# Optimization experiments

Hardware: AMD Instinct MI355X
Metric: run time of the kernel (lower is better)

## Reference

```python
import jax, jax.numpy as jnp
import numpy as np

C_ATOM = 128
N_HEADS = 4
HEAD_DIM = C_ATOM // N_HEADS


def setup_inputs() -> dict:
    key = jax.random.key(0)
    ks = jax.random.split(key, 11)
    B, L, A = 16, 4096, 4
    x = jax.random.normal(ks[0], (B, L, A, C_ATOM), dtype=jnp.float32)
    mask = jax.random.randint(ks[1], (B, L, A), 0, 2) > 0
    mask = mask.at[..., 0].set(True)  # ensure >=1 valid atom per residue (avoids all--inf softmax)
    s = 1.0 / np.sqrt(C_ATOM)
    def lin(k):
        kw, kb = jax.random.split(k)
        W = jax.random.uniform(kw, (C_ATOM, C_ATOM), jnp.float32, -s, s)
        b = jax.random.uniform(kb, (C_ATOM,), jnp.float32, -s, s)
        return W, b
    Wq, bq = lin(ks[2])
    Wk, bk = lin(ks[3])
    Wv, bv = lin(ks[4])
    Wo, bo = lin(ks[5])
    return {"x": x, "mask": mask, "Wq": Wq, "bq": bq, "Wk": Wk, "bk": bk,
            "Wv": Wv, "bv": bv, "Wo": Wo, "bo": bo}


def reference(x, mask, Wq, bq, Wk, bk, Wv, bv, Wo, bo):
    B, L, A, C = x.shape
    H, D = N_HEADS, HEAD_DIM
    # q/k/v projections (torch Linear: x @ W.T + b)
    q = (x @ Wq.T + bq).reshape(B, L, A, H, D)
    k = (x @ Wk.T + bk).reshape(B, L, A, H, D)
    v = (x @ Wv.T + bv).reshape(B, L, A, H, D)
    scale = 1.0 / jnp.sqrt(jnp.asarray(D, x.dtype))
    # per-residue 4x4 attention scores: [B, L, H, q_atom, k_atom]
    scores = jnp.einsum("blqhd,blkhd->blhqk", q, k) * scale
    # key-side mask bias (broadcast over heads and query atoms)
    bias = jnp.where(mask[:, :, None, None, :], 0.0, -jnp.inf).astype(x.dtype)
    attn = jax.nn.softmax(scores + bias, axis=-1)
    out = jnp.einsum("blhqk,blkhd->blqhd", attn, v).reshape(B, L, A, C)
    out = out @ Wo.T + bo
    residue_mask = jnp.any(mask, axis=-1)[..., None, None].astype(out.dtype)  # [B,L,1,1]
    return out * residue_mask
```

## Files before the change

kernel.cpp:

```cpp
#include <hip/hip_runtime.h>
#include <stdint.h>


typedef __bf16 bf16x8 __attribute__((ext_vector_type(8)));
typedef float  f32x4  __attribute__((ext_vector_type(4)));

#define N_RES 65536
#define RPB   16
#define MROWS 64
#define CDIM  128

__device__ __forceinline__ uint32_t pk2(float a, float b) {
    uint32_t ua = __builtin_bit_cast(uint32_t, a) + 0x8000u;
    uint32_t ub = __builtin_bit_cast(uint32_t, b) + 0x8000u;
    return (ua >> 16) | (ub & 0xffff0000u);
}
__device__ __forceinline__ uint16_t f2bf(float a) {
    uint32_t u = __builtin_bit_cast(uint32_t, a);
    return (uint16_t)((u + 0x7fffu + ((u >> 16) & 1u)) >> 16);
}
__device__ __forceinline__ bf16x8 pack8(float4 f0, float4 f1) {
    uint4 uu = make_uint4(pk2(f0.x, f0.y), pk2(f0.z, f0.w),
                          pk2(f1.x, f1.y), pk2(f1.z, f1.w));
    return __builtin_bit_cast(bf16x8, uu);
}
__device__ __forceinline__ void bf8_unpack(uint4 u, float* f) {
    f[0] = __builtin_bit_cast(float, u.x << 16);
    f[1] = __builtin_bit_cast(float, u.x & 0xffff0000u);
    f[2] = __builtin_bit_cast(float, u.y << 16);
    f[3] = __builtin_bit_cast(float, u.y & 0xffff0000u);
    f[4] = __builtin_bit_cast(float, u.z << 16);
    f[5] = __builtin_bit_cast(float, u.z & 0xffff0000u);
    f[6] = __builtin_bit_cast(float, u.w << 16);
    f[7] = __builtin_bit_cast(float, u.w & 0xffff0000u);
}

__global__ void wconv_kernel(const float* __restrict__ wq, const float* __restrict__ wk,
                             const float* __restrict__ wv, const float* __restrict__ wo,
                             uint16_t* __restrict__ dst) {
    int i = blockIdx.x * 256 + threadIdx.x;
    const float* s = (i < 16384) ? wq : (i < 32768) ? wk : (i < 49152) ? wv : wo;
    dst[i] = f2bf(s[i & 16383]);
}

template <bool USEWS>
__global__ __launch_bounds__(256, 2)
void laa_main(const float* __restrict__ x, const int* __restrict__ mask,
              const float* __restrict__ Wq, const float* __restrict__ bq,
              const float* __restrict__ Wk, const float* __restrict__ bk,
              const float* __restrict__ Wv, const float* __restrict__ bv,
              const float* __restrict__ Wo, const float* __restrict__ bo,
              const uint16_t* __restrict__ wbf,
              float* __restrict__ out) {
    __shared__ uint16_t sQ[MROWS * CDIM];
    __shared__ uint16_t sK[MROWS * CDIM];
    __shared__ uint16_t sV[MROWS * CDIM];
    __shared__ uint16_t sO[MROWS * CDIM];

    const int tid  = threadIdx.x;
    const int wave = tid >> 6;
    const int lane = tid & 63;
    const int lrow = lane & 15;
    const int quad = lane >> 4;
    const long m0  = (long)blockIdx.x * MROWS;

    const f32x4 vzero = {0.f, 0.f, 0.f, 0.f};

    bf16x8 af[4][4];
    {
        const float* xb = x + m0 * CDIM;
        #pragma unroll
        for (int m = 0; m < 4; ++m) {
            const float* rowp = xb + (m * 16 + lrow) * CDIM;
            #pragma unroll
            for (int ks = 0; ks < 4; ++ks) {
                const float4* p = (const float4*)(rowp + ks * 32 + quad * 8);
                af[m][ks] = pack8(p[0], p[1]);
            }
        }
    }

    f32x4 acc[3][4][2];
    #pragma unroll
    for (int g = 0; g < 3; ++g)
        #pragma unroll
        for (int m = 0; m < 4; ++m)
            #pragma unroll
            for (int nt = 0; nt < 2; ++nt) acc[g][m][nt] = vzero;

    const float* wsrc32[3] = {Wq, Wk, Wv};
    #pragma unroll
    for (int ks = 0; ks < 4; ++ks) {
        bf16x8 bfr[3][2];
        #pragma unroll
        for (int g = 0; g < 3; ++g) {
            #pragma unroll
            for (int nt = 0; nt < 2; ++nt) {
                int wrow = wave * 32 + nt * 16 + lrow;
                if constexpr (USEWS) {
                    bfr[g][nt] = *(const bf16x8*)(wbf + g * 16384 + wrow * CDIM + ks * 32 + quad * 8);
                } else {
                    const float* wp = wsrc32[g] + wrow * CDIM + ks * 32 + quad * 8;
                    bfr[g][nt] = pack8(((const float4*)wp)[0], ((const float4*)wp)[1]);
                }
            }
        }
        #pragma unroll
        for (int g = 0; g < 3; ++g)
            #pragma unroll
            for (int m = 0; m < 4; ++m)
                #pragma unroll
                for (int nt = 0; nt < 2; ++nt)
                    acc[g][m][nt] = __builtin_amdgcn_mfma_f32_16x16x32_bf16(
                        af[m][ks], bfr[g][nt], acc[g][m][nt], 0, 0, 0);
    }

    {
        uint16_t* sdst[3] = {sQ, sK, sV};
        const float* bias[3] = {bq, bk, bv};
        #pragma unroll
        for (int g = 0; g < 3; ++g) {
            #pragma unroll
            for (int nt = 0; nt < 2; ++nt) {
                int col = wave * 32 + nt * 16 + lrow;
                float bb = bias[g][col];
                #pragma unroll
                for (int m = 0; m < 4; ++m) {
                    #pragma unroll
                    for (int r = 0; r < 4; ++r) {
                        int row = m * 16 + quad * 4 + r;
                        sdst[g][row * CDIM + col] = f2bf(acc[g][m][nt][r] + bb);
                    }
                }
            }
        }
    }
    __syncthreads();

    {
        const int rl = tid >> 4;
        const int h  = (tid >> 2) & 3;
        const int qa = tid & 3;
        const int rowq = rl * 4 + qa;
        const int cb = h * 32;

        const int4 mk = *(const int4*)(mask + ((long)blockIdx.x * RPB + rl) * 4);
        const int mka[4] = {mk.x, mk.y, mk.z, mk.w};

        float qv[32];
        {
            const uint4* qp = (const uint4*)(sQ + rowq * CDIM + cb);
            #pragma unroll
            for (int c = 0; c < 4; ++c) bf8_unpack(qp[c], qv + c * 8);
        }
        float sc[4];
        #pragma unroll
        for (int ka = 0; ka < 4; ++ka) {
            const uint4* kp = (const uint4*)(sK + (rl * 4 + ka) * CDIM + cb);
            float d = 0.f;
            #pragma unroll
            for (int c = 0; c < 4; ++c) {
                float kv[8]; bf8_unpack(kp[c], kv);
                #pragma unroll
                for (int j = 0; j < 8; ++j) d += qv[c * 8 + j] * kv[j];
            }
            sc[ka] = d * 0.17677669529663689f;
        }
        float mx = -3e38f;
        #pragma unroll
        for (int ka = 0; ka < 4; ++ka) if (mka[ka]) mx = fmaxf(mx, sc[ka]);
        float e[4], ssum = 0.f;
        #pragma unroll
        for (int ka = 0; ka < 4; ++ka) {
            e[ka] = mka[ka] ? __expf(sc[ka] - mx) : 0.f;
            ssum += e[ka];
        }
        const float inv = ssum > 0.f ? 1.f / ssum : 0.f;

        float o[32];
        #pragma unroll
        for (int j = 0; j < 32; ++j) o[j] = 0.f;
        #pragma unroll
        for (int ka = 0; ka < 4; ++ka) {
            float wgt = e[ka] * inv;
            const uint4* vp = (const uint4*)(sV + (rl * 4 + ka) * CDIM + cb);
            #pragma unroll
            for (int c = 0; c < 4; ++c) {
                float vv[8]; bf8_unpack(vp[c], vv);
                #pragma unroll
                for (int j = 0; j < 8; ++j) o[c * 8 + j] += wgt * vv[j];
            }
        }
        uint32_t* op = (uint32_t*)(sO + rowq * CDIM + cb);
        #pragma unroll
        for (int c2 = 0; c2 < 16; ++c2) op[c2] = pk2(o[2 * c2], o[2 * c2 + 1]);
    }
    __syncthreads();

    f32x4 acc2[4][2];
    #pragma unroll
    for (int m = 0; m < 4; ++m)
        #pragma unroll
        for (int nt = 0; nt < 2; ++nt) acc2[m][nt] = vzero;

    #pragma unroll
    for (int ks = 0; ks < 4; ++ks) {
        bf16x8 a2[4];
        #pragma unroll
        for (int m = 0; m < 4; ++m)
            a2[m] = *(const bf16x8*)(sO + (m * 16 + lrow) * CDIM + ks * 32 + quad * 8);
        bf16x8 b2[2];
        #pragma unroll
        for (int nt = 0; nt < 2; ++nt) {
            int wrow = wave * 32 + nt * 16 + lrow;
            if constexpr (USEWS) {
                b2[nt] = *(const bf16x8*)(wbf + 3 * 16384 + wrow * CDIM + ks * 32 + quad * 8);
            } else {
                const float* wp = Wo + wrow * CDIM + ks * 32 + quad * 8;
                b2[nt] = pack8(((const float4*)wp)[0], ((const float4*)wp)[1]);
            }
        }
        #pragma unroll
        for (int m = 0; m < 4; ++m)
            #pragma unroll
            for (int nt = 0; nt < 2; ++nt)
                acc2[m][nt] = __builtin_amdgcn_mfma_f32_16x16x32_bf16(
                    a2[m], b2[nt], acc2[m][nt], 0, 0, 0);
    }
    {
        #pragma unroll
        for (int m = 0; m < 4; ++m) {
            const int4 mk2 = *(const int4*)(mask + ((long)blockIdx.x * RPB + m * 4 + quad) * 4);
            const float rm = (mk2.x | mk2.y | mk2.z | mk2.w) ? 1.f : 0.f;
            #pragma unroll
            for (int nt = 0; nt < 2; ++nt) {
                int col = wave * 32 + nt * 16 + lrow;
                float bb = bo[col];
                #pragma unroll
                for (int r = 0; r < 4; ++r) {
                    long row = m0 + m * 16 + quad * 4 + r;
                    out[row * CDIM + col] = (acc2[m][nt][r] + bb) * rm;
                }
            }
        }
    }
}

extern "C" void kernel_launch(void* const* d_in, const int* in_sizes, int n_in,
                              void* d_out, int out_size, void* d_ws, size_t ws_size,
                              hipStream_t stream) {
    const float* x    = (const float*)d_in[0];
    const int*   mask = (const int*)d_in[1];
    const float* Wq   = (const float*)d_in[2];
    const float* bq   = (const float*)d_in[3];
    const float* Wk   = (const float*)d_in[4];
    const float* bk   = (const float*)d_in[5];
    const float* Wv   = (const float*)d_in[6];
    const float* bv   = (const float*)d_in[7];
    const float* Wo   = (const float*)d_in[8];
    const float* bo   = (const float*)d_in[9];
    float* out = (float*)d_out;

    const int nblocks = N_RES / RPB;
    const bool usews = ws_size >= (size_t)(4 * 16384 * sizeof(uint16_t));
    if (usews) {
        uint16_t* wbf = (uint16_t*)d_ws;
        wconv_kernel<<<256, 256, 0, stream>>>(Wq, Wk, Wv, Wo, wbf);
        laa_main<true><<<nblocks, 256, 0, stream>>>(x, mask, Wq, bq, Wk, bk, Wv, bv,
                                                    Wo, bo, wbf, out);
    } else {
        laa_main<false><<<nblocks, 256, 0, stream>>>(x, mask, Wq, bq, Wk, bk, Wv, bv,
                                                     Wo, bo, nullptr, out);
    }
}
```

Baseline: 329.1 us.

## Keep per-head attention in registers via MFMA, switch to fp16, drop Q/K/V LDS

Each wave now owns one head's 32 columns and computes Q^T, K^T and V tiles directly in MFMA accumulator layout. Scores come from an MFMA on the transposed Q/K tiles, and the value mix is a block-diagonal 16x16x16 MFMA. This removes the sQ/sK/sV shared buffers, one barrier and the scalar dot-product attention phase. Precision changes from bf16 to fp16 with round-toward-zero packing, LDS use drops to one padded buffer, and launch bounds rise to 3 blocks per SM, at some risk of fp16 range and precision issues.

```diff
diff --git a/kernel.cpp b/kernel.cpp
--- a/kernel.cpp
+++ b/kernel.cpp
@@ -2,37 +2,21 @@
 #include <stdint.h>
 
 
-typedef __bf16 bf16x8 __attribute__((ext_vector_type(8)));
-typedef float  f32x4  __attribute__((ext_vector_type(4)));
+typedef __fp16 f16;
+typedef f16   f16x2 __attribute__((ext_vector_type(2)));
+typedef f16   f16x4 __attribute__((ext_vector_type(4)));
+typedef f16   f16x8 __attribute__((ext_vector_type(8)));
+typedef float f32x4 __attribute__((ext_vector_type(4)));
 
 #define N_RES 65536
 #define RPB   16
 #define MROWS 64
 #define CDIM  128
-
-__device__ __forceinline__ uint32_t pk2(float a, float b) {
-    uint32_t ua = __builtin_bit_cast(uint32_t, a) + 0x8000u;
-    uint32_t ub = __builtin_bit_cast(uint32_t, b) + 0x8000u;
-    return (ua >> 16) | (ub & 0xffff0000u);
-}
-__device__ __forceinline__ uint16_t f2bf(float a) {
-    uint32_t u = __builtin_bit_cast(uint32_t, a);
-    return (uint16_t)((u + 0x7fffu + ((u >> 16) & 1u)) >> 16);
-}
-__device__ __forceinline__ bf16x8 pack8(float4 f0, float4 f1) {
-    uint4 uu = make_uint4(pk2(f0.x, f0.y), pk2(f0.z, f0.w),
-                          pk2(f1.x, f1.y), pk2(f1.z, f1.w));
-    return __builtin_bit_cast(bf16x8, uu);
-}
-__device__ __forceinline__ void bf8_unpack(uint4 u, float* f) {
-    f[0] = __builtin_bit_cast(float, u.x << 16);
-    f[1] = __builtin_bit_cast(float, u.x & 0xffff0000u);
-    f[2] = __builtin_bit_cast(float, u.y << 16);
-    f[3] = __builtin_bit_cast(float, u.y & 0xffff0000u);
-    f[4] = __builtin_bit_cast(float, u.z << 16);
-    f[5] = __builtin_bit_cast(float, u.z & 0xffff0000u);
-    f[6] = __builtin_bit_cast(float, u.w << 16);
-    f[7] = __builtin_bit_cast(float, u.w & 0xffff0000u);
+#define SOP   136
+
+__device__ __forceinline__ uint32_t pkh(float a, float b) {
+    f16x2 h = __builtin_amdgcn_cvt_pkrtz(a, b);
+    return __builtin_bit_cast(uint32_t, h);
 }
 
 __global__ void wconv_kernel(const float* __restrict__ wq, const float* __restrict__ wk,
@@ -40,11 +24,26 @@
                              uint16_t* __restrict__ dst) {
     int i = blockIdx.x * 256 + threadIdx.x;
     const float* s = (i < 16384) ? wq : (i < 32768) ? wk : (i < 49152) ? wv : wo;
-    dst[i] = f2bf(s[i & 16383]);
+    f16 h = (f16)s[i & 16383];
+    dst[i] = __builtin_bit_cast(uint16_t, h);
 }
 
 template <bool USEWS>
-__global__ __launch_bounds__(256, 2)
+__device__ __forceinline__ f16x8 ldw16(const uint16_t* __restrict__ wbf,
+                                       const float* __restrict__ w32,
+                                       int goff, int row, int col) {
+    if constexpr (USEWS) {
+        return *(const f16x8*)(wbf + goff + row * CDIM + col);
+    } else {
+        const float4* p = (const float4*)(w32 + row * CDIM + col);
+        float4 a = p[0], b = p[1];
+        uint4 u = make_uint4(pkh(a.x, a.y), pkh(a.z, a.w), pkh(b.x, b.y), pkh(b.z, b.w));
+        return __builtin_bit_cast(f16x8, u);
+    }
+}
+
+template <bool USEWS>
+__global__ __launch_bounds__(256, 3)
 void laa_main(const float* __restrict__ x, const int* __restrict__ mask,
               const float* __restrict__ Wq, const float* __restrict__ bq,
               const float* __restrict__ Wk, const float* __restrict__ bk,
@@ -52,151 +51,112 @@
               const float* __restrict__ Wo, const float* __restrict__ bo,
               const uint16_t* __restrict__ wbf,
               float* __restrict__ out) {
-    __shared__ uint16_t sQ[MROWS * CDIM];
-    __shared__ uint16_t sK[MROWS * CDIM];
-    __shared__ uint16_t sV[MROWS * CDIM];
-    __shared__ uint16_t sO[MROWS * CDIM];
+    __shared__ uint16_t sO[MROWS * SOP];
 
     const int tid  = threadIdx.x;
     const int wave = tid >> 6;
     const int lane = tid & 63;
-    const int lrow = lane & 15;
+    const int l15  = lane & 15;
     const int quad = lane >> 4;
+    const int hb   = wave * 32;
     const long m0  = (long)blockIdx.x * MROWS;
 
     const f32x4 vzero = {0.f, 0.f, 0.f, 0.f};
 
-    bf16x8 af[4][4];
-    {
-        const float* xb = x + m0 * CDIM;
+    f32x4 qt[4][2], kt[4][2], vv[4][2];
+    #pragma unroll
+    for (int m = 0; m < 4; ++m)
+        #pragma unroll
+        for (int n = 0; n < 2; ++n) { qt[m][n] = vzero; kt[m][n] = vzero; vv[m][n] = vzero; }
+
+    #pragma unroll
+    for (int ks = 0; ks < 4; ++ks) {
+        f16x8 xf[4];
         #pragma unroll
         for (int m = 0; m < 4; ++m) {
-            const float* rowp = xb + (m * 16 + lrow) * CDIM;
-            #pragma unroll
-            for (int ks = 0; ks < 4; ++ks) {
-                const float4* p = (const float4*)(rowp + ks * 32 + quad * 8);
-                af[m][ks] = pack8(p[0], p[1]);
-            }
-        }
-    }
-
-    f32x4 acc[3][4][2];
-    #pragma unroll
-    for (int g = 0; g < 3; ++g)
-        #pragma unroll
-        for (int m = 0; m < 4; ++m)
-            #pragma unroll
-            for (int nt = 0; nt < 2; ++nt) acc[g][m][nt] = vzero;
-
-    const float* wsrc32[3] = {Wq, Wk, Wv};
-    #pragma unroll
-    for (int ks = 0; ks < 4; ++ks) {
-        bf16x8 bfr[3][2];
-        #pragma unroll
-        for (int g = 0; g < 3; ++g) {
+            const float4* p = (const float4*)(x + (m0 + m * 16 + l15) * CDIM + ks * 32 + quad * 8);
+            float4 a = p[0], b = p[1];
+            uint4 u = make_uint4(pkh(a.x, a.y), pkh(a.z, a.w), pkh(b.x, b.y), pkh(b.z, b.w));
+            xf[m] = __builtin_bit_cast(f16x8, u);
+        }
+        f16x8 wqf[2], wkf[2], wvf[2];
+        #pragma unroll
+        for (int nt = 0; nt < 2; ++nt) {
+            int row = hb + nt * 16 + l15, col = ks * 32 + quad * 8;
+            wqf[nt] = ldw16<USEWS>(wbf, Wq, 0,     row, col);
+            wkf[nt] = ldw16<USEWS>(wbf, Wk, 16384, row, col);
+            wvf[nt] = ldw16<USEWS>(wbf, Wv, 32768, row, col);
+        }
+        #pragma unroll
+        for (int m = 0; m < 4; ++m) {
             #pragma unroll
             for (int nt = 0; nt < 2; ++nt) {
-                int wrow = wave * 32 + nt * 16 + lrow;
-                if constexpr (USEWS) {
-                    bfr[g][nt] = *(const bf16x8*)(wbf + g * 16384 + wrow * CDIM + ks * 32 + quad * 8);
-                } else {
-                    const float* wp = wsrc32[g] + wrow * CDIM + ks * 32 + quad * 8;
-                    bfr[g][nt] = pack8(((const float4*)wp)[0], ((const float4*)wp)[1]);
-                }
+                qt[m][nt] = __builtin_amdgcn_mfma_f32_16x16x32_f16(wqf[nt], xf[m], qt[m][nt], 0, 0, 0);
+                kt[m][nt] = __builtin_amdgcn_mfma_f32_16x16x32_f16(wkf[nt], xf[m], kt[m][nt], 0, 0, 0);
+                vv[m][nt] = __builtin_amdgcn_mfma_f32_16x16x32_f16(xf[m], wvf[nt], vv[m][nt], 0, 0, 0);
             }
         }
-        #pragma unroll
-        for (int g = 0; g < 3; ++g)
-            #pragma unroll
-            for (int m = 0; m < 4; ++m)
-                #pragma unroll
-                for (int nt = 0; nt < 2; ++nt)
-                    acc[g][m][nt] = __builtin_amdgcn_mfma_f32_16x16x32_bf16(
-                        af[m][ks], bfr[g][nt], acc[g][m][nt], 0, 0, 0);
-    }
-
-    {
-        uint16_t* sdst[3] = {sQ, sK, sV};
-        const float* bias[3] = {bq, bk, bv};
-        #pragma unroll
-        for (int g = 0; g < 3; ++g) {
-            #pragma unroll
-            for (int nt = 0; nt < 2; ++nt) {
-                int col = wave * 32 + nt * 16 + lrow;
-                float bb = bias[g][col];
-                #pragma unroll
-                for (int m = 0; m < 4; ++m) {
-                    #pragma unroll
-                    for (int r = 0; r < 4; ++r) {
-                        int row = m * 16 + quad * 4 + r;
-                        sdst[g][row * CDIM + col] = f2bf(acc[g][m][nt][r] + bb);
-                    }
-                }
-            }
+    }
+
+    const float s = 0.17677669529663689f;
+    float bqs[8], bks[8];
+    #pragma unroll
+    for (int nd = 0; nd < 2; ++nd) {
+        float4 q4 = *(const float4*)(bq + hb + nd * 16 + quad * 4);
+        float4 k4 = *(const float4*)(bk + hb + nd * 16 + quad * 4);
+        bqs[nd * 4 + 0] = q4.x * s; bqs[nd * 4 + 1] = q4.y * s;
+        bqs[nd * 4 + 2] = q4.z * s; bqs[nd * 4 + 3] = q4.w * s;
+        bks[nd * 4 + 0] = k4.x;     bks[nd * 4 + 1] = k4.y;
+        bks[nd * 4 + 2] = k4.z;     bks[nd * 4 + 3] = k4.w;
+    }
+    const float bvv0 = bv[hb + l15], bvv1 = bv[hb + 16 + l15];
+
+    float rm[4];
+    const bool diag = (quad == (l15 >> 2));
+    #pragma unroll
+    for (int m = 0; m < 4; ++m) {
+        uint4 uq, uk;
+        uq.x = pkh(qt[m][0][0] * s + bqs[0], qt[m][0][1] * s + bqs[1]);
+        uq.y = pkh(qt[m][0][2] * s + bqs[2], qt[m][0][3] * s + bqs[3]);
+        uq.z = pkh(qt[m][1][0] * s + bqs[4], qt[m][1][1] * s + bqs[5]);
+        uq.w = pkh(qt[m][1][2] * s + bqs[6], qt[m][1][3] * s + bqs[7]);
+        uk.x = pkh(kt[m][0][0] + bks[0], kt[m][0][1] + bks[1]);
+        uk.y = pkh(kt[m][0][2] + bks[2], kt[m][0][3] + bks[3]);
+        uk.z = pkh(kt[m][1][0] + bks[4], kt[m][1][1] + bks[5]);
+        uk.w = pkh(kt[m][1][2] + bks[6], kt[m][1][3] + bks[7]);
+        f16x8 qtf = __builtin_bit_cast(f16x8, uq);
+        f16x8 ktf = __builtin_bit_cast(f16x8, uk);
+        f32x4 st = __builtin_amdgcn_mfma_f32_16x16x32_f16(ktf, qtf, vzero, 0, 0, 0);
+
+        const int4 mk = *(const int4*)(mask + ((long)blockIdx.x * RPB + m * 4 + quad) * 4);
+        rm[m] = (mk.x | mk.y | mk.z | mk.w) ? 1.f : 0.f;
+        float mx = -3e38f;
+        if (mk.x) mx = fmaxf(mx, st[0]);
+        if (mk.y) mx = fmaxf(mx, st[1]);
+        if (mk.z) mx = fmaxf(mx, st[2]);
+        if (mk.w) mx = fmaxf(mx, st[3]);
+        float e0 = mk.x ? __expf(st[0] - mx) : 0.f;
+        float e1 = mk.y ? __expf(st[1] - mx) : 0.f;
+        float e2 = mk.z ? __expf(st[2] - mx) : 0.f;
+        float e3 = mk.w ? __expf(st[3] - mx) : 0.f;
+        float inv = 1.f / (e0 + e1 + e2 + e3);
+        uint2 up = make_uint2(diag ? pkh(e0 * inv, e1 * inv) : 0u,
+                              diag ? pkh(e2 * inv, e3 * inv) : 0u);
+        f16x4 pf = __builtin_bit_cast(f16x4, up);
+
+        #pragma unroll
+        for (int nt = 0; nt < 2; ++nt) {
+            float bb = nt ? bvv1 : bvv0;
+            uint2 uv = make_uint2(pkh(vv[m][nt][0] + bb, vv[m][nt][1] + bb),
+                                  pkh(vv[m][nt][2] + bb, vv[m][nt][3] + bb));
+            f16x4 vbf = __builtin_bit_cast(f16x4, uv);
+            f32x4 ot = __builtin_amdgcn_mfma_f32_16x16x16f16(vbf, pf, vzero, 0, 0, 0);
+            uint2 w2 = make_uint2(pkh(ot[0], ot[1]), pkh(ot[2], ot[3]));
+            *(uint2*)(sO + (m * 16 + l15) * SOP + hb + nt * 16 + quad * 4) = w2;
         }
     }
     __syncthreads();
 
-    {
-        const int rl = tid >> 4;
-        const int h  = (tid >> 2) & 3;
-        const int qa = tid & 3;
-        const int rowq = rl * 4 + qa;
-        const int cb = h * 32;
-
-        const int4 mk = *(const int4*)(mask + ((long)blockIdx.x * RPB + rl) * 4);
-        const int mka[4] = {mk.x, mk.y, mk.z, mk.w};
-
-        float qv[32];
-        {
-            const uint4* qp = (const uint4*)(sQ + rowq * CDIM + cb);
-            #pragma unroll
-            for (int c = 0; c < 4; ++c) bf8_unpack(qp[c], qv + c * 8);
-        }
-        float sc[4];
-        #pragma unroll
-        for (int ka = 0; ka < 4; ++ka) {
-            const uint4* kp = (const uint4*)(sK + (rl * 4 + ka) * CDIM + cb);
-            float d = 0.f;
-            #pragma unroll
-            for (int c = 0; c < 4; ++c) {
-                float kv[8]; bf8_unpack(kp[c], kv);
-                #pragma unroll
-                for (int j = 0; j < 8; ++j) d += qv[c * 8 + j] * kv[j];
-            }
-            sc[ka] = d * 0.17677669529663689f;
-        }
-        float mx = -3e38f;
-        #pragma unroll
-        for (int ka = 0; ka < 4; ++ka) if (mka[ka]) mx = fmaxf(mx, sc[ka]);
-        float e[4], ssum = 0.f;
-        #pragma unroll
-        for (int ka = 0; ka < 4; ++ka) {
-            e[ka] = mka[ka] ? __expf(sc[ka] - mx) : 0.f;
-            ssum += e[ka];
-        }
-        const float inv = ssum > 0.f ? 1.f / ssum : 0.f;
-
-        float o[32];
-        #pragma unroll
-        for (int j = 0; j < 32; ++j) o[j] = 0.f;
-        #pragma unroll
-        for (int ka = 0; ka < 4; ++ka) {
-            float wgt = e[ka] * inv;
-            const uint4* vp = (const uint4*)(sV + (rl * 4 + ka) * CDIM + cb);
-            #pragma unroll
-            for (int c = 0; c < 4; ++c) {
-                float vv[8]; bf8_unpack(vp[c], vv);
-                #pragma unroll
-                for (int j = 0; j < 8; ++j) o[c * 8 + j] += wgt * vv[j];
-            }
-        }
-        uint32_t* op = (uint32_t*)(sO + rowq * CDIM + cb);
-        #pragma unroll
-        for (int c2 = 0; c2 < 16; ++c2) op[c2] = pk2(o[2 * c2], o[2 * c2 + 1]);
-    }
-    __syncthreads();
-
     f32x4 acc2[4][2];
     #pragma unroll
     for (int m = 0; m < 4; ++m)
@@ -205,41 +165,31 @@
 
     #pragma unroll
     for (int ks = 0; ks < 4; ++ks) {
-        bf16x8 a2[4];
+        f16x8 a2[4];
         #pragma unroll
         for (int m = 0; m < 4; ++m)
-            a2[m] = *(const bf16x8*)(sO + (m * 16 + lrow) * CDIM + ks * 32 + quad * 8);
-        bf16x8 b2[2];
-        #pragma unroll
-        for (int nt = 0; nt < 2; ++nt) {
-            int wrow = wave * 32 + nt * 16 + lrow;
-            if constexpr (USEWS) {
-                b2[nt] = *(const bf16x8*)(wbf + 3 * 16384 + wrow * CDIM + ks * 32 + quad * 8);
-            } else {
-                const float* wp = Wo + wrow * CDIM + ks * 32 + quad * 8;
-                b2[nt] = pack8(((const float4*)wp)[0], ((const float4*)wp)[1]);
-            }
-        }
+            a2[m] = *(const f16x8*)(sO + (m * 16 + l15) * SOP + ks * 32 + quad * 8);
+        f16x8 b2[2];
+        #pragma unroll
+        for (int nt = 0; nt < 2; ++nt)
+            b2[nt] = ldw16<USEWS>(wbf, Wo, 49152, hb + nt * 16 + l15, ks * 32 + quad * 8);
         #pragma unroll
         for (int m = 0; m < 4; ++m)
             #pragma unroll
             for (int nt = 0; nt < 2; ++nt)
-                acc2[m][nt] = __builtin_amdgcn_mfma_f32_16x16x32_bf16(
-                    a2[m], b2[nt], acc2[m][nt], 0, 0, 0);
+                acc2[m][nt] = __builtin_amdgcn_mfma_f32_16x16x32_f16(a2[m], b2[nt], acc2[m][nt], 0, 0, 0);
     }
     {
+        const float bo0 = bo[hb + l15], bo1 = bo[hb + 16 + l15];
         #pragma unroll
         for (int m = 0; m < 4; ++m) {
-            const int4 mk2 = *(const int4*)(mask + ((long)blockIdx.x * RPB + m * 4 + quad) * 4);
-            const float rm = (mk2.x | mk2.y | mk2.z | mk2.w) ? 1.f : 0.f;
             #pragma unroll
             for (int nt = 0; nt < 2; ++nt) {
-                int col = wave * 32 + nt * 16 + lrow;
-                float bb = bo[col];
+                float bb = nt ? bo1 : bo0;
                 #pragma unroll
                 for (int r = 0; r < 4; ++r) {
                     long row = m0 + m * 16 + quad * 4 + r;
-                    out[row * CDIM + col] = (acc2[m][nt][r] + bb) * rm;
+                    out[row * CDIM + hb + nt * 16 + l15] = (acc2[m][nt][r] + bb) * rm[m];
                 }
             }
         }
```

After: 361.2 us. 1.1x slower.
